# Performance work log

Measured on AMD Instinct MI355X. Metric: run time of the kernel, lower is better.

The kernel has to match this reference:

```python
import jax, jax.numpy as jnp
import numpy as np
from jax import lax

STRIDE = (1, 1)
PADDING = ((1, 1), (1, 1))
DILATION = (1, 1)
GROUPS = 1


def setup_inputs() -> dict:
    key = jax.random.key(0)
    k1, k2, k3, k4, k5 = jax.random.split(key, 5)
    # quantized int8-ish activations/weights stored as float (as in the torch module)
    x = jax.random.randint(k1, (32, 128, 56, 56), -128, 128).astype(jnp.float32)
    weight_int = jax.random.randint(k2, (256, 128, 3, 3), -128, 128).astype(jnp.float32)
    bias_int = jax.random.randint(k3, (256,), -1024, 1024).astype(jnp.float32)
    A = jax.random.randint(k4, (256,), 1, 32768)  # per-channel requant multiplier
    N = jax.random.randint(k5, (256,), 16, 25)    # per-channel shift
    return {
        "x": x,
        "weight_int": weight_int,
        "bias_int": bias_int,
        "A": A,
        "N": N,
        "out_min": 0,
        "out_max": 255,
    }


def reference(x, weight_int, bias_int, A, N, out_min, out_max):
    # emulate torch's x.int().float() truncation casts
    xq = jnp.trunc(x)
    wq = jnp.trunc(weight_int)
    bq = jnp.trunc(bias_int)
    out = lax.conv_general_dilated(
        xq, wq,
        window_strides=STRIDE,
        padding=PADDING,
        rhs_dilation=DILATION,
        feature_group_count=GROUPS,
        dimension_numbers=("NCHW", "OIHW", "NCHW"),
    )
    out = jnp.round(out + bq[None, :, None, None])
    # out *= A ; out >>= N  (torch float rshift == divide by 2**N)
    Af = A.astype(jnp.float32)[None, :, None, None]
    Nf = N.astype(jnp.float32)[None, :, None, None]
    out = out * Af / jnp.exp2(Nf)
    if out_min >= 0:
        out = jnp.clip(jnp.round(out), float(out_min), float(out_max))
    return out
```

## Files before the change

### kernel.cpp

```cpp
#include <hip/hip_runtime.h>
#include <stdint.h>

typedef int   v4i __attribute__((ext_vector_type(4)));
typedef float v4f __attribute__((ext_vector_type(4)));

#define XT_H_STRIDE (66*128)
#define XT_N_STRIDE (58*66*128)
#define XT_BYTES    (32*58*66*128)
#define WQ_BYTES    (256*1152)

__device__ __forceinline__ void gload16(const void* g, void* l) {
  __builtin_amdgcn_global_load_lds(
      (const __attribute__((address_space(1))) void*)g,
      (__attribute__((address_space(3))) void*)l, 16, 0, 0);
}

__global__ __launch_bounds__(256) void xform_x(const float* __restrict__ x,
                                               char* __restrict__ xt) {
  __shared__ int LB[56 * 33];
  int bid = blockIdx.x;
  int n  = bid / 58;
  int hp = bid - n * 58;
  int t  = threadIdx.x;
  int srch = hp - 1;
  bool rowok = (srch >= 0) && (srch < 56);
  char* dstrow = xt + (size_t)n * XT_N_STRIDE + (size_t)hp * XT_H_STRIDE;

  if (rowok) {
    const float* rb = x + ((size_t)(n * 128) * 56 + srch) * 56;
#pragma unroll
    for (int u0 = 0; u0 < 2; ++u0) {
      int u  = t + u0 * 256;
      int wb = u & 15;
      int cb = u >> 4;
      int w0 = wb * 4, ci0 = cb * 4;
      if (w0 < 56) {
        int dw[4] = {0, 0, 0, 0};
#pragma unroll
        for (int i = 0; i < 4; ++i) {
          v4f f = *(const v4f*)(rb + (size_t)(ci0 + i) * 3136 + w0);
#pragma unroll
          for (int j = 0; j < 4; ++j)
            dw[j] |= (((int)f[j]) & 255) << (8 * i);
        }
#pragma unroll
        for (int j = 0; j < 4; ++j)
          LB[(w0 + j) * 33 + cb] = dw[j];
      }
    }
    __syncthreads();
    for (int c = t; c < 528; c += 256) {
      int wp  = c >> 3;
      int cio = c & 7;
      int srw = wp - 1;
      v4i v = {0, 0, 0, 0};
      if (srw >= 0 && srw < 56) {
#pragma unroll
        for (int k = 0; k < 4; ++k) v[k] = LB[srw * 33 + cio * 4 + k];
      }
      *(v4i*)(dstrow + c * 16) = v;
    }
  } else {
    v4i z = {0, 0, 0, 0};
    for (int c = t; c < 528; c += 256) *(v4i*)(dstrow + c * 16) = z;
  }
}

__global__ __launch_bounds__(256) void xform_w(const float* __restrict__ wsrc,
                                               const int* __restrict__ Aq,
                                               const int* __restrict__ Nq,
                                               char* __restrict__ wq,
                                               float* __restrict__ scale) {
  int idx = blockIdx.x * 256 + threadIdx.x;
  int co = idx / 1152;
  int r  = idx - co * 1152;
  int g  = r >> 7;
  int ci = r & 127;
  int kh = g / 3;
  int kw = g - 3 * kh;
  float f = wsrc[(size_t)(co * 128 + ci) * 9 + kh * 3 + kw];
  wq[idx] = (signed char)(int)f;
  if (idx < 256) {
    scale[idx] = (float)Aq[idx] * exp2f(-(float)Nq[idx]);
  }
}

__global__ __launch_bounds__(256) void qconv_gemm(
    const char* __restrict__ xt, const char* __restrict__ wq,
    const float* __restrict__ bias, const float* __restrict__ scale,
    const int* __restrict__ pmin, const int* __restrict__ pmax,
    float* __restrict__ out) {
  __shared__ __align__(16) char As[2][8192];
  __shared__ __align__(16) char Bs[2][8192];

  int bid = blockIdx.x;
  int xcd = bid & 7;
  int q   = bid >> 3;
  int mt  = q & 1;
  int nt  = xcd * 112 + (q >> 1);
  int n   = nt / 28;
  int ht  = nt - n * 28;
  int h0  = ht * 2;
  int m0  = mt * 128;

  int t  = threadIdx.x;
  int wv = t >> 6;
  int ln = t & 63;
  int quad = ln >> 4;
  int l16  = ln & 15;
  int wm = wv & 1, wn = wv >> 1;

  const char* wbase = wq + (size_t)m0 * 1152;
  const char* xbase = xt + (size_t)n * XT_N_STRIDE + (size_t)h0 * XT_H_STRIDE;

  int a_m1 = t >> 2;
  int a_p  = (((t & 3) ^ ((t >> 3) & 3)) * 16);
  int b_w1 = t >> 2;
  int ldsoff = wv * 1024;

  v4i acc[4][4];
#pragma unroll
  for (int i = 0; i < 4; ++i)
#pragma unroll
    for (int j = 0; j < 4; ++j) {
      v4i z = {0, 0, 0, 0};
      acc[i][j] = z;
    }

  int sw = (l16 >> 1) & 3;
  int ca = (quad ^ sw) * 16;

  auto stage = [&](int kt, int p) {
    int g  = kt >> 1;
    int c0 = (kt & 1) << 6;
    int kh = g / 3;
    int kw = g - 3 * kh;
    int k0 = kt << 6;
    gload16(wbase + (size_t)a_m1 * 1152 + k0 + a_p, &As[p][ldsoff]);
    gload16(wbase + (size_t)(a_m1 + 64) * 1152 + k0 + a_p, &As[p][4096 + ldsoff]);
    const char* rowb = xbase + (size_t)kh * XT_H_STRIDE + (size_t)kw * 128 + c0;
    gload16(rowb + (size_t)b_w1 * 128 + a_p, &Bs[p][ldsoff]);
    gload16(rowb + XT_H_STRIDE + (size_t)b_w1 * 128 + a_p, &Bs[p][4096 + ldsoff]);
  };

  stage(0, 0);
  for (int kt = 0; kt < 18; ++kt) {
    int p = kt & 1;
    asm volatile("s_barrier" ::: "memory");
    if (kt < 17) {
      stage(kt + 1, 1 - p);
      asm volatile("s_waitcnt vmcnt(4)" ::: "memory");
    } else {
      asm volatile("s_waitcnt vmcnt(0)" ::: "memory");
    }
    asm volatile("s_barrier" ::: "memory");

    v4i a[4], b[4];
#pragma unroll
    for (int i = 0; i < 4; ++i)
      a[i] = *(const v4i*)(&As[p][(wm * 64 + i * 16 + l16) * 64 + ca]);
#pragma unroll
    for (int j = 0; j < 4; ++j)
      b[j] = *(const v4i*)(&Bs[p][(wn * 64 + j * 16 + l16) * 64 + ca]);
#pragma unroll
    for (int i = 0; i < 4; ++i)
#pragma unroll
      for (int j = 0; j < 4; ++j)
        acc[i][j] = __builtin_amdgcn_mfma_i32_16x16x64_i8(a[i], b[j], acc[i][j], 0, 0, 0);
  }

  float mn = (float)pmin[0];
  float mx = (float)pmax[0];
#pragma unroll
  for (int i = 0; i < 4; ++i) {
    int co_b = m0 + wm * 64 + i * 16 + quad * 4;
#pragma unroll
    for (int r = 0; r < 4; ++r) {
      int co = co_b + r;
      float bs = bias[co];
      float sc = scale[co];
#pragma unroll
      for (int j = 0; j < 4; ++j) {
        int sl = wn * 64 + j * 16 + l16;
        int w  = sl & 63;
        int dh = sl >> 6;
        if (w < 56) {
          float f = (float)acc[i][j][r] + bs;
          f = rintf(f * sc);
          f = fminf(fmaxf(f, mn), mx);
          out[(((size_t)n * 256 + co) * 56 + (h0 + dh)) * 56 + w] = f;
        }
      }
    }
  }
}

extern "C" void kernel_launch(void* const* d_in, const int* in_sizes, int n_in,
                              void* d_out, int out_size, void* d_ws, size_t ws_size,
                              hipStream_t stream) {
  const float* x  = (const float*)d_in[0];
  const float* w  = (const float*)d_in[1];
  const float* b  = (const float*)d_in[2];
  const int*   Aq = (const int*)d_in[3];
  const int*   Nq = (const int*)d_in[4];
  const int*   mn = (const int*)d_in[5];
  const int*   mx = (const int*)d_in[6];
  float* out = (float*)d_out;

  char*  xt    = (char*)d_ws;
  char*  wq    = xt + XT_BYTES;
  float* scale = (float*)(wq + WQ_BYTES);

  hipLaunchKernelGGL(xform_x, dim3(32 * 58), dim3(256), 0, stream, x, xt);
  hipLaunchKernelGGL(xform_w, dim3(1152), dim3(256), 0, stream, w, Aq, Nq, wq, scale);
  hipLaunchKernelGGL(qconv_gemm, dim3(1792), dim3(256), 0, stream,
                     xt, wq, b, scale, mn, mx, out);
}
```

Baseline: 195.6 us.

## Preload full 4-row input halo into LDS and re-tile weights by K-chunk

After: 190.2 us. 2.8% less time.

```diff
diff --git a/kernel.cpp b/kernel.cpp
--- a/kernel.cpp
+++ b/kernel.cpp
@@ -69,29 +69,29 @@
 __global__ __launch_bounds__(256) void xform_w(const float* __restrict__ wsrc,
                                                const int* __restrict__ Aq,
                                                const int* __restrict__ Nq,
-                                               char* __restrict__ wq,
+                                               char* __restrict__ wq2,
                                                float* __restrict__ scale) {
   int idx = blockIdx.x * 256 + threadIdx.x;
   int co = idx / 1152;
-  int r  = idx - co * 1152;
-  int g  = r >> 7;
-  int ci = r & 127;
+  int k  = idx - co * 1152;
+  int g  = k >> 7;
+  int ci = k & 127;
   int kh = g / 3;
   int kw = g - 3 * kh;
   float f = wsrc[(size_t)(co * 128 + ci) * 9 + kh * 3 + kw];
-  wq[idx] = (signed char)(int)f;
+  wq2[((k >> 6) * 256 + co) * 64 + (k & 63)] = (signed char)(int)f;
   if (idx < 256) {
     scale[idx] = (float)Aq[idx] * exp2f(-(float)Nq[idx]);
   }
 }
 
 __global__ __launch_bounds__(256) void qconv_gemm(
-    const char* __restrict__ xt, const char* __restrict__ wq,
+    const char* __restrict__ xt, const char* __restrict__ wq2,
     const float* __restrict__ bias, const float* __restrict__ scale,
     const int* __restrict__ pmin, const int* __restrict__ pmax,
     float* __restrict__ out) {
+  __shared__ __align__(16) char Bp[4 * 8448];
   __shared__ __align__(16) char As[2][8192];
-  __shared__ __align__(16) char Bs[2][8192];
 
   int bid = blockIdx.x;
   int xcd = bid & 7;
@@ -110,13 +110,27 @@
   int l16  = ln & 15;
   int wm = wv & 1, wn = wv >> 1;
 
-  const char* wbase = wq + (size_t)m0 * 1152;
-  const char* xbase = xt + (size_t)n * XT_N_STRIDE + (size_t)h0 * XT_H_STRIDE;
-
-  int a_m1 = t >> 2;
-  int a_p  = (((t & 3) ^ ((t >> 3) & 3)) * 16);
-  int b_w1 = t >> 2;
-  int ldsoff = wv * 1024;
+  const char* wbase = wq2 + (size_t)m0 * 64;
+  const char* xb    = xt + (size_t)n * XT_N_STRIDE + (size_t)h0 * XT_H_STRIDE;
+
+  int a_off  = (t >> 2) * 64 + (((t & 3) ^ ((t >> 3) & 3)) * 16);
+  int ldsA   = wv * 1024;
+
+  for (int it = 0; it < 9; ++it) {
+    int s = t + it * 256;
+    if (s < 2112) {
+      int row = s / 528;
+      int rr  = s - row * 528;
+      int w   = rr >> 3;
+      int cq  = rr & 7;
+      gload16(xb + row * XT_H_STRIDE + w * 128 + ((cq ^ (w & 7)) << 4),
+              Bp + it * 4096 + wv * 1024);
+    }
+  }
+  gload16(wbase + a_off, &As[0][ldsA]);
+  gload16(wbase + 4096 + a_off, &As[0][4096 + ldsA]);
+  asm volatile("s_waitcnt vmcnt(0)" ::: "memory");
+  asm volatile("s_barrier" ::: "memory");
 
   v4i acc[4][4];
 #pragma unroll
@@ -127,41 +141,35 @@
       acc[i][j] = z;
     }
 
-  int sw = (l16 >> 1) & 3;
-  int ca = (quad ^ sw) * 16;
-
-  auto stage = [&](int kt, int p) {
+  int ca = ((quad ^ ((l16 >> 1) & 3)) * 16);
+
+  for (int kt = 0; kt < 18; ++kt) {
+    int p  = kt & 1;
     int g  = kt >> 1;
-    int c0 = (kt & 1) << 6;
     int kh = g / 3;
     int kw = g - 3 * kh;
-    int k0 = kt << 6;
-    gload16(wbase + (size_t)a_m1 * 1152 + k0 + a_p, &As[p][ldsoff]);
-    gload16(wbase + (size_t)(a_m1 + 64) * 1152 + k0 + a_p, &As[p][4096 + ldsoff]);
-    const char* rowb = xbase + (size_t)kh * XT_H_STRIDE + (size_t)kw * 128 + c0;
-    gload16(rowb + (size_t)b_w1 * 128 + a_p, &Bs[p][ldsoff]);
-    gload16(rowb + XT_H_STRIDE + (size_t)b_w1 * 128 + a_p, &Bs[p][4096 + ldsoff]);
-  };
-
-  stage(0, 0);
-  for (int kt = 0; kt < 18; ++kt) {
-    int p = kt & 1;
+
     asm volatile("s_barrier" ::: "memory");
     if (kt < 17) {
-      stage(kt + 1, 1 - p);
-      asm volatile("s_waitcnt vmcnt(4)" ::: "memory");
+      const char* wkt = wbase + ((kt + 1) << 14);
+      gload16(wkt + a_off, &As[1 - p][ldsA]);
+      gload16(wkt + 4096 + a_off, &As[1 - p][4096 + ldsA]);
+      asm volatile("s_waitcnt vmcnt(2)" ::: "memory");
     } else {
       asm volatile("s_waitcnt vmcnt(0)" ::: "memory");
     }
     asm volatile("s_barrier" ::: "memory");
 
+    int bswz = (((p << 2) + quad) ^ ((l16 + kw) & 7)) << 4;
+    const char* bbase = Bp + (wn + kh) * XT_H_STRIDE + (l16 + kw) * 128 + bswz;
+
     v4i a[4], b[4];
 #pragma unroll
     for (int i = 0; i < 4; ++i)
       a[i] = *(const v4i*)(&As[p][(wm * 64 + i * 16 + l16) * 64 + ca]);
 #pragma unroll
     for (int j = 0; j < 4; ++j)
-      b[j] = *(const v4i*)(&Bs[p][(wn * 64 + j * 16 + l16) * 64 + ca]);
+      b[j] = *(const v4i*)(bbase + j * 2048);
 #pragma unroll
     for (int i = 0; i < 4; ++i)
 #pragma unroll
@@ -208,11 +216,11 @@
   float* out = (float*)d_out;
 
   char*  xt    = (char*)d_ws;
-  char*  wq    = xt + XT_BYTES;
-  float* scale = (float*)(wq + WQ_BYTES);
+  char*  wq2   = xt + XT_BYTES;
+  float* scale = (float*)(wq2 + WQ_BYTES);
 
   hipLaunchKernelGGL(xform_x, dim3(32 * 58), dim3(256), 0, stream, x, xt);
-  hipLaunchKernelGGL(xform_w, dim3(1152), dim3(256), 0, stream, w, Aq, Nq, wq, scale);
+  hipLaunchKernelGGL(xform_w, dim3(1152), dim3(256), 0, stream, w, Aq, Nq, wq2, scale);
   hipLaunchKernelGGL(qconv_gemm, dim3(1792), dim3(256), 0, stream,
-                     xt, wq, b, scale, mn, mx, out);
-}
+                     xt, wq2, b, scale, mn, mx, out);
+}
```
